# Performance work log

Measured on AMD Instinct MI355X. Metric: run time of the kernel, lower is better.

## Reference

```python
import jax, jax.numpy as jnp
import numpy as np

RC = 5.0                 # cutoff radius (init kwarg)
B, M = 128, 256          # structures per batch, atoms per structure
L = 17.2                 # box edge (Angstrom) -> ~0.05 atoms/A^3, ~27 nbrs/atom at rc=5
P = 2_097_152            # fixed max pair count (output padding)


def _pairs(coord):
    """Cell-list candidate generation + radius filter, batched over structures.

    Faithful to the TF CellListNL (no 'cell' / open-boundary path): atoms are
    shifted to the positive octant, binned into cells of edge rc, and candidate
    pairs are atoms of the same structure whose cell bins differ by at most 1 in
    every dimension (the 27-cell stencil). Final pairs satisfy 0 < dist < rc.
    """
    pos = coord - jnp.min(coord, axis=0)                          # [N,3] shift (as in TF code)
    cell = jnp.floor(pos / RC).astype(jnp.int32)                  # [N,3] cell bins
    posb = pos.reshape(B, M, 3)
    cellb = cell.reshape(B, M, 3)
    diff = posb[:, None, :, :] - posb[:, :, None, :]              # [B,M,M,3] = pos_j - pos_i
    sq = jnp.sum(diff * diff, axis=-1)                            # [B,M,M]
    nz = sq > 0.0
    dist = jnp.sqrt(jnp.where(nz, sq, 1.0)) * nz                  # safe norm (0 on diagonal)
    # 27-neighbor-cell stencil == per-axis bin difference in {-1,0,1}
    nbr = jnp.all(jnp.abs(cellb[:, None, :, :] - cellb[:, :, None, :]) <= 1, axis=-1)
    mask = nbr & (dist < RC) & nz                                 # [B,M,M]
    return diff, dist, mask


def setup_inputs() -> dict:
    key = jax.random.key(0)
    coord = jax.random.uniform(key, (B * M, 3), jnp.float32) * L  # atoms in [0,L)^3 per structure
    ind_1 = jnp.repeat(jnp.arange(B, dtype=jnp.int32), M)         # structure index per atom
    return {"coord": coord, "ind_1": ind_1}


def reference(coord, ind_1):
    # ind_1 is encoded structurally: atoms are laid out as B contiguous blocks of M,
    # so same-structure pairing is enforced by the batched [B,M,M] computation.
    diff, dist, mask = _pairs(coord)
    b, i, j = jnp.nonzero(mask, size=P, fill_value=0)             # fixed-size pair list
    valid = mask[b, i, j]                                         # False on padded rows
    d = dist[b, i, j] * valid                                     # [P]
    df = diff[b, i, j] * valid[:, None]                           # [P,3]
    ind_2 = jnp.stack([b * M + i, b * M + j], axis=1) * valid[:, None].astype(jnp.int32)
    return ind_2, d, df
```

## Files before the change

kernel.cpp:

```cpp
#include <hip/hip_runtime.h>

#define BB 128
#define MM 256
#define NN (BB * MM)
#define PP 2097152
#define RCF 5.0f
#define NBLK 512
#define GTH (NBLK * 256)
#define CAP 2048

typedef unsigned long long u64;


__global__ void __launch_bounds__(256)
min_k(const float* __restrict__ coord, float* __restrict__ partials) {
    const int g = blockIdx.x * 256 + threadIdx.x;
    float x = coord[3 * g + 0];
    float y = coord[3 * g + 1];
    float z = coord[3 * g + 2];
    #pragma unroll
    for (int off = 32; off > 0; off >>= 1) {
        x = fminf(x, __shfl_xor(x, off, 64));
        y = fminf(y, __shfl_xor(y, off, 64));
        z = fminf(z, __shfl_xor(z, off, 64));
    }
    __shared__ float lx[4], ly[4], lz[4];
    const int w = threadIdx.x >> 6;
    if ((threadIdx.x & 63) == 0) { lx[w] = x; ly[w] = y; lz[w] = z; }
    __syncthreads();
    if (threadIdx.x == 0) {
        partials[3 * blockIdx.x + 0] = fminf(fminf(lx[0], lx[1]), fminf(lx[2], lx[3]));
        partials[3 * blockIdx.x + 1] = fminf(fminf(ly[0], ly[1]), fminf(ly[2], ly[3]));
        partials[3 * blockIdx.x + 2] = fminf(fminf(lz[0], lz[1]), fminf(lz[2], lz[3]));
    }
}

__device__ inline void reduce_min128(const float* __restrict__ partials,
                                     float& mnx, float& mny, float& mnz) {
    const int lane = threadIdx.x & 63;
    float x = fminf(partials[3 * lane + 0], partials[3 * (lane + 64) + 0]);
    float y = fminf(partials[3 * lane + 1], partials[3 * (lane + 64) + 1]);
    float z = fminf(partials[3 * lane + 2], partials[3 * (lane + 64) + 2]);
    #pragma unroll
    for (int off = 32; off > 0; off >>= 1) {
        x = fminf(x, __shfl_xor(x, off, 64));
        y = fminf(y, __shfl_xor(y, off, 64));
        z = fminf(z, __shfl_xor(z, off, 64));
    }
    mnx = x; mny = y; mnz = z;
}


__global__ void __launch_bounds__(256)
count_k(const float* __restrict__ coord, const float* __restrict__ partials,
        u64* __restrict__ masks, int* __restrict__ bsums) {
    const int b2 = blockIdx.x;
    const int b = b2 >> 2, rblk = b2 & 3;
    const int t = threadIdx.x;
    const int lane = t & 63, w = t >> 6;
    float mnx, mny, mnz;
    reduce_min128(partials, mnx, mny, mnz);

    __shared__ float sx[4][65], sy[4][65], sz[4][65];
    __shared__ int wsum[4];
    const int ja = b * MM + t;
    sx[t >> 6][t & 63] = __fsub_rn(coord[3 * ja + 0], mnx);
    sy[t >> 6][t & 63] = __fsub_rn(coord[3 * ja + 1], mny);
    sz[t >> 6][t & 63] = __fsub_rn(coord[3 * ja + 2], mnz);
    __syncthreads();

    const int i_loc = t >> 2, c = t & 3;
    const float pix = sx[rblk][i_loc], piy = sy[rblk][i_loc], piz = sz[rblk][i_loc];
    u64 m = 0ULL;
    for (int jj = 0; jj < 64; ++jj) {
        float dx = __fsub_rn(sx[c][jj], pix);
        float dy = __fsub_rn(sy[c][jj], piy);
        float dz = __fsub_rn(sz[c][jj], piz);
        float sq = __fadd_rn(__fadd_rn(__fmul_rn(dx, dx), __fmul_rn(dy, dy)),
                             __fmul_rn(dz, dz));
        if (sq > 0.0f && __fsqrt_rn(sq) < RCF) m |= (1ULL << jj);
    }
    masks[b2 * 256 + t] = m;

    int v = __popcll(m);
    #pragma unroll
    for (int off = 32; off > 0; off >>= 1) v += __shfl_xor(v, off, 64);
    if (lane == 0) wsum[w] = v;
    __syncthreads();
    if (t == 0) bsums[b2] = wsum[0] + wsum[1] + wsum[2] + wsum[3];
}

__device__ inline void zero_range(float* __restrict__ o, int lo, int hi, int g) {
    int a = (lo + 3) & ~3;
    if (a > hi) a = hi;
    if (g < a - lo) o[lo + g] = 0.0f;
    float4* o4 = reinterpret_cast<float4*>(o);
    const float4 z4 = make_float4(0.f, 0.f, 0.f, 0.f);
    for (int q = (a >> 2) + g; q < (hi >> 2); q += GTH) o4[q] = z4;
}

__global__ void __launch_bounds__(256)
write_k(const float* __restrict__ coord, const float* __restrict__ partials,
        const u64* __restrict__ masks, const int* __restrict__ bsums,
        float* __restrict__ outF) {
    const int b2 = blockIdx.x;
    const int b = b2 >> 2, rblk = b2 & 3;
    const int t = threadIdx.x;
    const int lane = t & 63, w = t >> 6;
    float mnx, mny, mnz;
    reduce_min128(partials, mnx, mny, mnz);

    __shared__ float sx[4][65], sy[4][65], sz[4][65];
    __shared__ int tmp[256];
    __shared__ int pre[NBLK];
    __shared__ int sTotS;
    __shared__ int wsum[4];
    __shared__ float sd[CAP];
    __shared__ float sind[2 * CAP];
    __shared__ float sdf[3 * CAP];

    const int ja = b * MM + t;
    sx[t >> 6][t & 63] = __fsub_rn(coord[3 * ja + 0], mnx);
    sy[t >> 6][t & 63] = __fsub_rn(coord[3 * ja + 1], mny);
    sz[t >> 6][t & 63] = __fsub_rn(coord[3 * ja + 2], mnz);

    const int v0 = bsums[2 * t], v1 = bsums[2 * t + 1];
    const int s01 = v0 + v1;
    tmp[t] = s01;
    __syncthreads();
    #pragma unroll
    for (int off = 1; off < 256; off <<= 1) {
        int v = (t >= off) ? tmp[t - off] : 0;
        __syncthreads();
        tmp[t] += v;
        __syncthreads();
    }
    const int excl = tmp[t] - s01;
    pre[2 * t] = excl;
    pre[2 * t + 1] = excl + v0;
    if (t == 255) sTotS = excl + s01;
    __syncthreads();

    const int base = pre[b2];
    const int total = (sTotS < PP) ? sTotS : PP;

    const u64 mask = masks[b2 * 256 + t];
    const int cnt = __popcll(mask);
    int incl = cnt;
    #pragma unroll
    for (int off = 1; off < 64; off <<= 1) {
        int v = __shfl_up(incl, off, 64);
        if (lane >= off) incl += v;
    }
    if (lane == 63) wsum[w] = incl;
    __syncthreads();
    const int agg = wsum[0] + wsum[1] + wsum[2] + wsum[3];
    int woff = 0;
    for (int k = 0; k < w; ++k) woff += wsum[k];
    const int lexcl = woff + incl - cnt;

    const int i_loc = t >> 2, c = t & 3;
    const float pix = sx[rblk][i_loc], piy = sy[rblk][i_loc], piz = sz[rblk][i_loc];
    const int gi = b * MM + rblk * 64 + i_loc;
    const int gj0 = b * MM + c * 64;

    const int nbat = (agg + CAP - 1) / CAP;
    for (int bb = 0; bb < nbat; ++bb) {
        const int wlo = bb * CAP, whi = wlo + CAP;
        int q = lexcl;
        u64 mm = mask;
        while (mm) {
            const int jj = __ffsll((long long)mm) - 1;
            mm &= mm - 1;
            if (q >= whi) break;
            if (q >= wlo) {
                float dx = __fsub_rn(sx[c][jj], pix);
                float dy = __fsub_rn(sy[c][jj], piy);
                float dz = __fsub_rn(sz[c][jj], piz);
                float sq = __fadd_rn(__fadd_rn(__fmul_rn(dx, dx), __fmul_rn(dy, dy)),
                                     __fmul_rn(dz, dz));
                const int s = q - wlo;
                sd[s] = __fsqrt_rn(sq);
                sind[2 * s + 0] = (float)gi;
                sind[2 * s + 1] = (float)(gj0 + jj);
                sdf[3 * s + 0] = dx;
                sdf[3 * s + 1] = dy;
                sdf[3 * s + 2] = dz;
            }
            q++;
        }
        __syncthreads();
        const int nq = ((agg - wlo) < CAP) ? (agg - wlo) : CAP;
        const int pbase = base + wlo;
        int rem = PP - pbase; if (rem < 0) rem = 0;
        const int nv = (nq < rem) ? nq : rem;
        for (int k = t; k < nv; k += 256)     outF[2 * PP + pbase + k]     = sd[k];
        for (int k = t; k < 2 * nv; k += 256) outF[2 * pbase + k]          = sind[k];
        for (int k = t; k < 3 * nv; k += 256) outF[3 * PP + 3 * pbase + k] = sdf[k];
        __syncthreads();
    }

    const int g = b2 * 256 + t;
    zero_range(outF, 2 * total,          2 * PP, g);
    zero_range(outF, 2 * PP + total,     3 * PP, g);
    zero_range(outF, 3 * PP + 3 * total, 6 * PP, g);
}

extern "C" void kernel_launch(void* const* d_in, const int* in_sizes, int n_in,
                              void* d_out, int out_size, void* d_ws, size_t ws_size,
                              hipStream_t stream) {
    const float* coord = (const float*)d_in[0];
    float* outF = (float*)d_out;

    u64*   masks    = (u64*)d_ws;
    int*   bsums    = (int*)(masks + GTH);
    float* partials = (float*)(bsums + NBLK);

    min_k  <<<128,  256, 0, stream>>>(coord, partials);
    count_k<<<NBLK, 256, 0, stream>>>(coord, partials, masks, bsums);
    write_k<<<NBLK, 256, 0, stream>>>(coord, partials, masks, bsums, outF);
}
```

Measured before the change: 32.36 us.

## Fuse global min into count kernel and streamline scan and tile layout

Removes the separate min_k launch: every count_k block now recomputes the global coordinate minimum redundantly using float4 loads over the whole 384 KB coordinate array, and block 0 writes it out for write_k. Replaces sqrt-compare with a squared-distance threshold constant, packs tiles into float4 shared arrays, and replaces the multi-sync block scan of bsums with a single-wave shuffle scan. This saves a launch and several barriers, at the cost of each of the 512 blocks reading all coordinates (mostly from L2).

Result: faster. 31.26 us (-3.4%).

```diff
diff --git a/kernel.cpp b/kernel.cpp
--- a/kernel.cpp
+++ b/kernel.cpp
@@ -1,93 +1,23 @@
 #include <hip/hip_runtime.h>
-
-#define BB 128
+#include <float.h>
+
 #define MM 256
-#define NN (BB * MM)
 #define PP 2097152
-#define RCF 5.0f
 #define NBLK 512
 #define GTH (NBLK * 256)
 #define CAP 2048
+#define SQMAX 24.999996185302734375f
 
 typedef unsigned long long u64;
 
 
-__global__ void __launch_bounds__(256)
-min_k(const float* __restrict__ coord, float* __restrict__ partials) {
-    const int g = blockIdx.x * 256 + threadIdx.x;
-    float x = coord[3 * g + 0];
-    float y = coord[3 * g + 1];
-    float z = coord[3 * g + 2];
+__device__ inline void wave_min3(float& x, float& y, float& z) {
     #pragma unroll
     for (int off = 32; off > 0; off >>= 1) {
         x = fminf(x, __shfl_xor(x, off, 64));
         y = fminf(y, __shfl_xor(y, off, 64));
         z = fminf(z, __shfl_xor(z, off, 64));
     }
-    __shared__ float lx[4], ly[4], lz[4];
-    const int w = threadIdx.x >> 6;
-    if ((threadIdx.x & 63) == 0) { lx[w] = x; ly[w] = y; lz[w] = z; }
-    __syncthreads();
-    if (threadIdx.x == 0) {
-        partials[3 * blockIdx.x + 0] = fminf(fminf(lx[0], lx[1]), fminf(lx[2], lx[3]));
-        partials[3 * blockIdx.x + 1] = fminf(fminf(ly[0], ly[1]), fminf(ly[2], ly[3]));
-        partials[3 * blockIdx.x + 2] = fminf(fminf(lz[0], lz[1]), fminf(lz[2], lz[3]));
-    }
-}
-
-__device__ inline void reduce_min128(const float* __restrict__ partials,
-                                     float& mnx, float& mny, float& mnz) {
-    const int lane = threadIdx.x & 63;
-    float x = fminf(partials[3 * lane + 0], partials[3 * (lane + 64) + 0]);
-    float y = fminf(partials[3 * lane + 1], partials[3 * (lane + 64) + 1]);
-    float z = fminf(partials[3 * lane + 2], partials[3 * (lane + 64) + 2]);
-    #pragma unroll
-    for (int off = 32; off > 0; off >>= 1) {
-        x = fminf(x, __shfl_xor(x, off, 64));
-        y = fminf(y, __shfl_xor(y, off, 64));
-        z = fminf(z, __shfl_xor(z, off, 64));
-    }
-    mnx = x; mny = y; mnz = z;
-}
-
-
-__global__ void __launch_bounds__(256)
-count_k(const float* __restrict__ coord, const float* __restrict__ partials,
-        u64* __restrict__ masks, int* __restrict__ bsums) {
-    const int b2 = blockIdx.x;
-    const int b = b2 >> 2, rblk = b2 & 3;
-    const int t = threadIdx.x;
-    const int lane = t & 63, w = t >> 6;
-    float mnx, mny, mnz;
-    reduce_min128(partials, mnx, mny, mnz);
-
-    __shared__ float sx[4][65], sy[4][65], sz[4][65];
-    __shared__ int wsum[4];
-    const int ja = b * MM + t;
-    sx[t >> 6][t & 63] = __fsub_rn(coord[3 * ja + 0], mnx);
-    sy[t >> 6][t & 63] = __fsub_rn(coord[3 * ja + 1], mny);
-    sz[t >> 6][t & 63] = __fsub_rn(coord[3 * ja + 2], mnz);
-    __syncthreads();
-
-    const int i_loc = t >> 2, c = t & 3;
-    const float pix = sx[rblk][i_loc], piy = sy[rblk][i_loc], piz = sz[rblk][i_loc];
-    u64 m = 0ULL;
-    for (int jj = 0; jj < 64; ++jj) {
-        float dx = __fsub_rn(sx[c][jj], pix);
-        float dy = __fsub_rn(sy[c][jj], piy);
-        float dz = __fsub_rn(sz[c][jj], piz);
-        float sq = __fadd_rn(__fadd_rn(__fmul_rn(dx, dx), __fmul_rn(dy, dy)),
-                             __fmul_rn(dz, dz));
-        if (sq > 0.0f && __fsqrt_rn(sq) < RCF) m |= (1ULL << jj);
-    }
-    masks[b2 * 256 + t] = m;
-
-    int v = __popcll(m);
-    #pragma unroll
-    for (int off = 32; off > 0; off >>= 1) v += __shfl_xor(v, off, 64);
-    if (lane == 0) wsum[w] = v;
-    __syncthreads();
-    if (t == 0) bsums[b2] = wsum[0] + wsum[1] + wsum[2] + wsum[3];
 }
 
 __device__ inline void zero_range(float* __restrict__ o, int lo, int hi, int g) {
@@ -99,50 +29,108 @@
     for (int q = (a >> 2) + g; q < (hi >> 2); q += GTH) o4[q] = z4;
 }
 
+
 __global__ void __launch_bounds__(256)
-write_k(const float* __restrict__ coord, const float* __restrict__ partials,
+count_k(const float* __restrict__ coord, float* __restrict__ minvec,
+        u64* __restrict__ masks, int* __restrict__ bsums) {
+    const int b2 = blockIdx.x;
+    const int b = b2 >> 2, rblk = b2 & 3;
+    const int t = threadIdx.x;
+    const int lane = t & 63, w = t >> 6;
+
+    __shared__ float4 tile4[4][65];
+    __shared__ float lmin[3][4];
+    __shared__ int wsum[4];
+
+    const float4* c4 = reinterpret_cast<const float4*>(coord);
+    float mx = FLT_MAX, my = FLT_MAX, mz = FLT_MAX;
+    #pragma unroll 4
+    for (int k = 0; k < 32; ++k) {
+        const int basei = (k * 256 + t) * 3;
+        const float4 f0 = c4[basei + 0];
+        const float4 f1 = c4[basei + 1];
+        const float4 f2 = c4[basei + 2];
+        mx = fminf(mx, fminf(fminf(f0.x, f0.w), fminf(f1.z, f2.y)));
+        my = fminf(my, fminf(fminf(f0.y, f1.x), fminf(f1.w, f2.z)));
+        mz = fminf(mz, fminf(fminf(f0.z, f1.y), fminf(f2.x, f2.w)));
+    }
+    wave_min3(mx, my, mz);
+    if (lane == 0) { lmin[0][w] = mx; lmin[1][w] = my; lmin[2][w] = mz; }
+    __syncthreads();
+    mx = fminf(fminf(lmin[0][0], lmin[0][1]), fminf(lmin[0][2], lmin[0][3]));
+    my = fminf(fminf(lmin[1][0], lmin[1][1]), fminf(lmin[1][2], lmin[1][3]));
+    mz = fminf(fminf(lmin[2][0], lmin[2][1]), fminf(lmin[2][2], lmin[2][3]));
+    if (b2 == 0 && t == 0) { minvec[0] = mx; minvec[1] = my; minvec[2] = mz; }
+
+    const int ja = b * MM + t;
+    tile4[w][lane] = make_float4(__fsub_rn(coord[3 * ja + 0], mx),
+                                 __fsub_rn(coord[3 * ja + 1], my),
+                                 __fsub_rn(coord[3 * ja + 2], mz), 0.0f);
+    __syncthreads();
+
+    const int i_loc = t >> 2, c = t & 3;
+    const float4 pi4 = tile4[rblk][i_loc];
+    u64 m = 0ULL;
+    for (int jj = 0; jj < 64; ++jj) {
+        float4 v = tile4[c][jj];
+        float dx = __fsub_rn(v.x, pi4.x);
+        float dy = __fsub_rn(v.y, pi4.y);
+        float dz = __fsub_rn(v.z, pi4.z);
+        float sq = __fadd_rn(__fadd_rn(__fmul_rn(dx, dx), __fmul_rn(dy, dy)),
+                             __fmul_rn(dz, dz));
+        if (sq > 0.0f && sq <= SQMAX) m |= (1ULL << jj);
+    }
+    masks[b2 * 256 + t] = m;
+
+    int v = __popcll(m);
+    #pragma unroll
+    for (int off = 32; off > 0; off >>= 1) v += __shfl_xor(v, off, 64);
+    if (lane == 0) wsum[w] = v;
+    __syncthreads();
+    if (t == 0) bsums[b2] = wsum[0] + wsum[1] + wsum[2] + wsum[3];
+}
+
+__global__ void __launch_bounds__(256)
+write_k(const float* __restrict__ coord, const float* __restrict__ minvec,
         const u64* __restrict__ masks, const int* __restrict__ bsums,
         float* __restrict__ outF) {
     const int b2 = blockIdx.x;
     const int b = b2 >> 2, rblk = b2 & 3;
     const int t = threadIdx.x;
     const int lane = t & 63, w = t >> 6;
-    float mnx, mny, mnz;
-    reduce_min128(partials, mnx, mny, mnz);
-
-    __shared__ float sx[4][65], sy[4][65], sz[4][65];
-    __shared__ int tmp[256];
+
+    __shared__ float4 tile4[4][65];
     __shared__ int pre[NBLK];
-    __shared__ int sTotS;
+    __shared__ int sTot;
     __shared__ int wsum[4];
     __shared__ float sd[CAP];
     __shared__ float sind[2 * CAP];
     __shared__ float sdf[3 * CAP];
 
+    const float mnx = minvec[0], mny = minvec[1], mnz = minvec[2];
     const int ja = b * MM + t;
-    sx[t >> 6][t & 63] = __fsub_rn(coord[3 * ja + 0], mnx);
-    sy[t >> 6][t & 63] = __fsub_rn(coord[3 * ja + 1], mny);
-    sz[t >> 6][t & 63] = __fsub_rn(coord[3 * ja + 2], mnz);
-
-    const int v0 = bsums[2 * t], v1 = bsums[2 * t + 1];
-    const int s01 = v0 + v1;
-    tmp[t] = s01;
-    __syncthreads();
-    #pragma unroll
-    for (int off = 1; off < 256; off <<= 1) {
-        int v = (t >= off) ? tmp[t - off] : 0;
-        __syncthreads();
-        tmp[t] += v;
-        __syncthreads();
-    }
-    const int excl = tmp[t] - s01;
-    pre[2 * t] = excl;
-    pre[2 * t + 1] = excl + v0;
-    if (t == 255) sTotS = excl + s01;
-    __syncthreads();
-
+    tile4[w][lane] = make_float4(__fsub_rn(coord[3 * ja + 0], mnx),
+                                 __fsub_rn(coord[3 * ja + 1], mny),
+                                 __fsub_rn(coord[3 * ja + 2], mnz), 0.0f);
+
+    if (w == 0) {
+        int v[8]; int s = 0;
+        #pragma unroll
+        for (int q = 0; q < 8; ++q) { v[q] = bsums[lane * 8 + q]; s += v[q]; }
+        int isum = s;
+        #pragma unroll
+        for (int off = 1; off < 64; off <<= 1) {
+            int u = __shfl_up(isum, off, 64);
+            if (lane >= off) isum += u;
+        }
+        int run = isum - s;
+        #pragma unroll
+        for (int q = 0; q < 8; ++q) { pre[lane * 8 + q] = run; run += v[q]; }
+        if (lane == 63) sTot = run;
+    }
+    __syncthreads();
     const int base = pre[b2];
-    const int total = (sTotS < PP) ? sTotS : PP;
+    const int total = (sTot < PP) ? sTot : PP;
 
     const u64 mask = masks[b2 * 256 + t];
     const int cnt = __popcll(mask);
@@ -160,7 +148,7 @@
     const int lexcl = woff + incl - cnt;
 
     const int i_loc = t >> 2, c = t & 3;
-    const float pix = sx[rblk][i_loc], piy = sy[rblk][i_loc], piz = sz[rblk][i_loc];
+    const float4 pi4 = tile4[rblk][i_loc];
     const int gi = b * MM + rblk * 64 + i_loc;
     const int gj0 = b * MM + c * 64;
 
@@ -174,9 +162,10 @@
             mm &= mm - 1;
             if (q >= whi) break;
             if (q >= wlo) {
-                float dx = __fsub_rn(sx[c][jj], pix);
-                float dy = __fsub_rn(sy[c][jj], piy);
-                float dz = __fsub_rn(sz[c][jj], piz);
+                float4 v = tile4[c][jj];
+                float dx = __fsub_rn(v.x, pi4.x);
+                float dy = __fsub_rn(v.y, pi4.y);
+                float dz = __fsub_rn(v.z, pi4.z);
                 float sq = __fadd_rn(__fadd_rn(__fmul_rn(dx, dx), __fmul_rn(dy, dy)),
                                      __fmul_rn(dz, dz));
                 const int s = q - wlo;
@@ -212,11 +201,10 @@
     const float* coord = (const float*)d_in[0];
     float* outF = (float*)d_out;
 
-    u64*   masks    = (u64*)d_ws;
-    int*   bsums    = (int*)(masks + GTH);
-    float* partials = (float*)(bsums + NBLK);
-
-    min_k  <<<128,  256, 0, stream>>>(coord, partials);
-    count_k<<<NBLK, 256, 0, stream>>>(coord, partials, masks, bsums);
-    write_k<<<NBLK, 256, 0, stream>>>(coord, partials, masks, bsums, outF);
-}
+    u64*   masks  = (u64*)d_ws;
+    int*   bsums  = (int*)(masks + GTH);
+    float* minvec = (float*)(bsums + NBLK);
+
+    count_k<<<NBLK, 256, 0, stream>>>(coord, minvec, masks, bsums);
+    write_k<<<NBLK, 256, 0, stream>>>(coord, minvec, masks, bsums, outF);
+}
```
